# Performance work log

Hardware: AMD Instinct MI355X
Metric: run time of the kernel (lower is better)

The kernel has to match this reference:

```python
import jax, jax.numpy as jnp
import numpy as np

B, S, HID = 2, 2048, 2048
NH, NKV, D = 16, 8, 128
EPS = 1e-6
THETA = 10000.0


def _rms_norm(x, w):
    # RMSNorm over last dim (head_dim), Qwen3-style per-head q/k norm
    var = jnp.mean(jnp.square(x), axis=-1, keepdims=True)
    return x * jax.lax.rsqrt(var + EPS) * w


def _rotate_half(x):
    x1, x2 = jnp.split(x, 2, axis=-1)
    return jnp.concatenate([-x2, x1], axis=-1)


def setup_inputs() -> dict:
    key = jax.random.key(0)
    ks = jax.random.split(key, 8)
    hidden_states = jax.random.normal(ks[0], (B, S, HID), dtype=jnp.float32)
    # rotary embeddings (HF-style: emb = concat(freqs, freqs))
    inv_freq = 1.0 / (THETA ** (jnp.arange(0, D, 2, dtype=jnp.float32) / D))
    pos = jnp.arange(S, dtype=jnp.float32)
    freqs = jnp.outer(pos, inv_freq)                      # [S, D/2]
    emb = jnp.concatenate([freqs, freqs], axis=-1)        # [S, D]
    cos = jnp.broadcast_to(jnp.cos(emb)[None], (B, S, D))
    sin = jnp.broadcast_to(jnp.sin(emb)[None], (B, S, D))
    w_scale = 1.0 / np.sqrt(HID)
    Wq = jax.random.normal(ks[1], (HID, NH * D), dtype=jnp.float32) * w_scale
    Wk = jax.random.normal(ks[2], (HID, NKV * D), dtype=jnp.float32) * w_scale
    Wv = jax.random.normal(ks[3], (HID, NKV * D), dtype=jnp.float32) * w_scale
    Wo = jax.random.normal(ks[4], (NH * D, HID), dtype=jnp.float32) * w_scale
    q_norm_w = jnp.ones((D,), dtype=jnp.float32)
    k_norm_w = jnp.ones((D,), dtype=jnp.float32)
    return {"hidden_states": hidden_states, "cos": cos, "sin": sin,
            "Wq": Wq, "Wk": Wk, "Wv": Wv, "Wo": Wo,
            "q_norm_w": q_norm_w, "k_norm_w": k_norm_w}


def reference(hidden_states, cos, sin, Wq, Wk, Wv, Wo, q_norm_w, k_norm_w):
    b, s, _ = hidden_states.shape
    # projections + per-head RMSNorm on q/k, then [B,H,S,D]
    q = _rms_norm((hidden_states @ Wq).reshape(b, s, NH, D), q_norm_w)
    k = _rms_norm((hidden_states @ Wk).reshape(b, s, NKV, D), k_norm_w)
    v = (hidden_states @ Wv).reshape(b, s, NKV, D)
    q = jnp.swapaxes(q, 1, 2)  # [B,NH,S,D]
    k = jnp.swapaxes(k, 1, 2)  # [B,NKV,S,D]
    v = jnp.swapaxes(v, 1, 2)
    # rotary position embedding
    c = cos[:, None, :, :]
    sn = sin[:, None, :, :]
    q = q * c + _rotate_half(q) * sn
    k = k * c + _rotate_half(k) * sn
    # GQA: expand kv heads to match query heads
    rep = NH // NKV
    k = jnp.repeat(k, rep, axis=1)
    v = jnp.repeat(v, rep, axis=1)
    # scaled causal attention (splash_attention semantics, causal mask)
    q = q * (D ** -0.5)
    scores = jnp.einsum('bhqd,bhkd->bhqk', q, k)
    causal = jnp.tril(jnp.ones((s, s), dtype=bool))
    scores = jnp.where(causal[None, None], scores, jnp.finfo(scores.dtype).min)
    attn = jax.nn.softmax(scores, axis=-1)
    out = jnp.einsum('bhqk,bhkd->bhqd', attn, v)
    out = jnp.swapaxes(out, 1, 2).reshape(b, s, NH * D)
    return out @ Wo
```

## Files before the change

### kernel.cpp

```cpp
#include <hip/hip_runtime.h>
#include <hip/hip_bf16.h>

typedef unsigned short u16;
typedef unsigned int u32;
typedef unsigned long long u64;
typedef __attribute__((ext_vector_type(8))) short short8;
typedef __attribute__((ext_vector_type(4))) float floatx4;

#define AS1 __attribute__((address_space(1)))
#define AS3 __attribute__((address_space(3)))

__device__ __forceinline__ float bf2f(u16 u) {
    u32 x = ((u32)u) << 16;
    float f;
    __builtin_memcpy(&f, &x, 4);
    return f;
}
__device__ __forceinline__ u16 f2bf(float f) {
    u32 x;
    __builtin_memcpy(&x, &f, 4);
    u32 r = (x + 0x7fffu + ((x >> 16) & 1u)) >> 16;
    return (u16)r;
}
__device__ __forceinline__ u32 f2bf_pk(float a, float b) {
    __hip_bfloat162 h = __float22bfloat162_rn(float2{a, b});
    u32 r;
    __builtin_memcpy(&r, &h, 4);
    return r;
}

__global__ __launch_bounds__(256) void convert_x(const float* __restrict__ in,
                                                 u16* __restrict__ out) {
    int i = blockIdx.x * 256 + threadIdx.x;
    float4 v = *(const float4*)(in + (size_t)i * 4);
    u16 o[4] = {f2bf(v.x), f2bf(v.y), f2bf(v.z), f2bf(v.w)};
    *(u64*)(out + (size_t)i * 4) = *(u64*)o;
}

__global__ __launch_bounds__(1024) void transpose_wall(const float* __restrict__ Wq,
                                                       const float* __restrict__ Wk,
                                                       const float* __restrict__ Wv,
                                                       const float* __restrict__ Wo,
                                                       u16* __restrict__ WqkvT,
                                                       u16* __restrict__ WoT) {
    const int z = blockIdx.z;
    const float* in;
    u16* out;
    int C;
    if (z == 0) { in = Wq; out = WqkvT; C = 2048; }
    else if (z == 1) { in = Wk; out = WqkvT + 2048 * 2048; C = 1024; }
    else if (z == 2) { in = Wv; out = WqkvT + 3072 * 2048; C = 1024; }
    else { in = Wo; out = WoT; C = 2048; }
    const int c0 = blockIdx.x * 32, r0 = blockIdx.y * 32;
    if (c0 >= C) return;
    __shared__ u16 t[32][33];
    const int tx = threadIdx.x, ty = threadIdx.y;
    t[ty][tx] = f2bf(in[(size_t)(r0 + ty) * C + c0 + tx]);
    __syncthreads();
    out[(size_t)(c0 + ty) * 2048 + r0 + tx] = t[tx][ty];
}

__global__ __launch_bounds__(1024) void transpose_v(const u16* __restrict__ QKV,
                                                    u16* __restrict__ Vt) {
    __shared__ u16 t[32][33];
    const int tx = threadIdx.x, ty = threadIdx.y;
    const int b = blockIdx.z >> 3, kv = blockIdx.z & 7;
    const int s0 = blockIdx.x * 32, d0 = blockIdx.y * 32;
    t[ty][tx] = QKV[(size_t)(b * 2048 + s0 + ty) * 4096 + 3072 + kv * 128 + d0 + tx];
    __syncthreads();
    Vt[(size_t)((b * 8 + kv) * 128 + d0 + ty) * 2048 + s0 + tx] = t[tx][ty];
}

template <typename OUT_T>
__global__ __launch_bounds__(512, 2) void gemm256(const u16* __restrict__ A,
                                                  const u16* __restrict__ Bt,
                                                  OUT_T* __restrict__ C,
                                                  int M, int N, int K) {
    (void)M;
    __shared__ __align__(16) u16 lds[2][2][2][128 * 64];
    const int tid = threadIdx.x;
    const int wave = tid >> 6, lane = tid & 63;
    const int lr = lane & 15, lq = lane >> 4;
    const int wm = wave >> 2, wn = wave & 3;
    const int m0 = blockIdx.y * 256, n0 = blockIdx.x * 256;

    const int srow = lane >> 3;
    const int schunk = ((lane & 7) ^ srow) << 3;
    const int slot = wave << 1;

    auto stage = [&](const u16* src, int rbase, int buf, int mat, int half, int k0) {
#pragma unroll
        for (int j = 0; j < 2; j++) {
            int r = rbase + half * 128 + (slot + j) * 8 + srow;
            __builtin_amdgcn_global_load_lds(
                (const AS1 void*)(src + (size_t)r * K + k0 + schunk),
                (AS3 void*)(&lds[buf][mat][half][(slot + j) * 512]), 16, 0, 0);
        }
    };

    floatx4 zf = {0.f, 0.f, 0.f, 0.f};
    floatx4 acc[8][4];
#pragma unroll
    for (int i = 0; i < 8; i++)
#pragma unroll
        for (int jn = 0; jn < 4; jn++) acc[i][jn] = zf;

    const int NT = K >> 6;

    stage(Bt, n0, 0, 1, 0, 0);
    stage(Bt, n0, 0, 1, 1, 0);
    stage(A, m0, 0, 0, 0, 0);
    stage(A, m0, 0, 0, 1, 0);
    if (NT > 1) {
        stage(Bt, n0, 1, 1, 0, 64);
        stage(Bt, n0, 1, 1, 1, 64);
        stage(A, m0, 1, 0, 0, 64);
        asm volatile("s_waitcnt vmcnt(6)" ::: "memory");
    } else {
        asm volatile("s_waitcnt vmcnt(0)" ::: "memory");
    }
    __builtin_amdgcn_s_barrier();

    for (int kt = 0; kt < NT; kt++) {
        const int b = kt & 1;
        const u16* Ab = &lds[b][0][wm][0];
        const u16* Bb = &lds[b][1][wn >> 1][0];
        const int brow = (wn & 1) * 64;
        const int sx = lr & 7;
        const int nk = (kt + 2) << 6;

        short8 bf0[4], bf1[4], af[4];
#pragma unroll
        for (int jn = 0; jn < 4; jn++) {
            int rh = brow + jn * 16 + lr;
            bf0[jn] = *(const short8*)(Bb + rh * 64 + ((lq ^ sx) << 3));
            bf1[jn] = *(const short8*)(Bb + rh * 64 + (((4 + lq) ^ sx) << 3));
        }
#pragma unroll
        for (int i = 0; i < 4; i++)
            af[i] = *(const short8*)(Ab + (i * 16 + lr) * 64 + ((lq ^ sx) << 3));
        if (kt + 1 < NT) stage(A, m0, b ^ 1, 0, 1, (kt + 1) << 6);
        __builtin_amdgcn_s_barrier();
        asm volatile("s_waitcnt lgkmcnt(0)" ::: "memory");
        __builtin_amdgcn_sched_barrier(0);
        __builtin_amdgcn_s_setprio(1);
#pragma unroll
        for (int i = 0; i < 4; i++)
#pragma unroll
            for (int jn = 0; jn < 4; jn++)
                acc[i][jn] = __builtin_amdgcn_mfma_f32_16x16x32_bf16(af[i], bf0[jn], acc[i][jn], 0, 0, 0);
        __builtin_amdgcn_s_setprio(0);
        __builtin_amdgcn_s_barrier();

        short8 ag[4];
#pragma unroll
        for (int i = 0; i < 4; i++)
            ag[i] = *(const short8*)(Ab + ((i + 4) * 16 + lr) * 64 + ((lq ^ sx) << 3));
        if (kt + 2 < NT) stage(Bt, n0, b, 1, 0, nk);
        __builtin_amdgcn_s_barrier();
        asm volatile("s_waitcnt lgkmcnt(0)" ::: "memory");
        __builtin_amdgcn_sched_barrier(0);
        __builtin_amdgcn_s_setprio(1);
#pragma unroll
        for (int i = 0; i < 4; i++)
#pragma unroll
            for (int jn = 0; jn < 4; jn++)
                acc[i + 4][jn] = __builtin_amdgcn_mfma_f32_16x16x32_bf16(ag[i], bf0[jn], acc[i + 4][jn], 0, 0, 0);
        __builtin_amdgcn_s_setprio(0);
        __builtin_amdgcn_s_barrier();

        short8 c0[4], c1[4];
#pragma unroll
        for (int i = 0; i < 4; i++) {
            c0[i] = *(const short8*)(Ab + (i * 16 + lr) * 64 + (((4 + lq) ^ sx) << 3));
            c1[i] = *(const short8*)(Ab + ((i + 4) * 16 + lr) * 64 + (((4 + lq) ^ sx) << 3));
        }
        if (kt + 2 < NT) stage(Bt, n0, b, 1, 1, nk);
        __builtin_amdgcn_s_barrier();
        asm volatile("s_waitcnt lgkmcnt(0)" ::: "memory");
        __builtin_amdgcn_sched_barrier(0);
        __builtin_amdgcn_s_setprio(1);
#pragma unroll
        for (int i = 0; i < 4; i++)
#pragma unroll
            for (int jn = 0; jn < 4; jn++)
                acc[i][jn] = __builtin_amdgcn_mfma_f32_16x16x32_bf16(c0[i], bf1[jn], acc[i][jn], 0, 0, 0);
        __builtin_amdgcn_s_setprio(0);
        __builtin_amdgcn_s_barrier();

        if (kt + 2 < NT) stage(A, m0, b, 0, 0, nk);
        __builtin_amdgcn_s_barrier();
        __builtin_amdgcn_s_setprio(1);
#pragma unroll
        for (int i = 0; i < 4; i++)
#pragma unroll
            for (int jn = 0; jn < 4; jn++)
                acc[i + 4][jn] = __builtin_amdgcn_mfma_f32_16x16x32_bf16(c1[i], bf1[jn], acc[i + 4][jn], 0, 0, 0);
        __builtin_amdgcn_s_setprio(0);
        if (kt + 2 < NT) asm volatile("s_waitcnt vmcnt(6)" ::: "memory");
        else asm volatile("s_waitcnt vmcnt(0)" ::: "memory");
        __builtin_amdgcn_s_barrier();
    }

#pragma unroll
    for (int i = 0; i < 8; i++)
#pragma unroll
        for (int jn = 0; jn < 4; jn++)
#pragma unroll
            for (int r = 0; r < 4; r++) {
                int row = m0 + wm * 128 + i * 16 + lq * 4 + r;
                int col = n0 + wn * 64 + jn * 16 + lr;
                if constexpr (sizeof(OUT_T) == 2)
                    C[(size_t)row * N + col] = f2bf(acc[i][jn][r]);
                else
                    C[(size_t)row * N + col] = acc[i][jn][r];
            }
}

__global__ __launch_bounds__(256) void norm_rope(u16* __restrict__ QKV,
                                                 const float* __restrict__ cosb,
                                                 const float* __restrict__ sinb,
                                                 const float* __restrict__ qw,
                                                 const float* __restrict__ kw) {
    const int tid = threadIdx.x;
    const int wave = tid >> 6, lane = tid & 63;
    const int t = blockIdx.x * 4 + wave;
    u16* ptr;
    const float* w;
    float scale;
    int bs;
    if (t < 65536) {
        bs = t >> 4;
        ptr = QKV + (size_t)bs * 4096 + (t & 15) * 128;
        w = qw;
        scale = 0.08838834764831845f * 1.4426950408889634f;
    } else {
        int t2 = t - 65536;
        bs = t2 >> 3;
        ptr = QKV + (size_t)bs * 4096 + 2048 + (t2 & 7) * 128;
        w = kw;
        scale = 1.0f;
    }
    const int d = lane * 2;
    u32 xv = *(const u32*)(ptr + d);
    float x0 = bf2f((u16)(xv & 0xffff)), x1 = bf2f((u16)(xv >> 16));
    float ss = x0 * x0 + x1 * x1;
#pragma unroll
    for (int off = 1; off < 64; off <<= 1) ss += __shfl_xor(ss, off);
    float rn = rsqrtf(ss * (1.0f / 128.0f) + 1e-6f);
    float2 wv = *(const float2*)(w + d);
    float y0 = x0 * rn * wv.x;
    float y1 = x1 * rn * wv.y;
    float p0 = __shfl_xor(y0, 32);
    float p1 = __shfl_xor(y1, 32);
    float sgn = (lane < 32) ? -1.0f : 1.0f;
    float2 cv = *(const float2*)(cosb + (size_t)bs * 128 + d);
    float2 sv = *(const float2*)(sinb + (size_t)bs * 128 + d);
    float o0 = (y0 * cv.x + sgn * p0 * sv.x) * scale;
    float o1 = (y1 * cv.y + sgn * p1 * sv.y) * scale;
    *(u32*)(ptr + d) = (u32)f2bf(o0) | ((u32)f2bf(o1) << 16);
}

__global__ __launch_bounds__(512, 2) void attn_kernel(const u16* __restrict__ QKV,
                                                      const u16* __restrict__ Vt,
                                                      u16* __restrict__ O) {
    __shared__ __align__(16) u16 Ks[2][64 * 128];
    __shared__ __align__(16) u16 Vs[2][128 * 64];
    const int tid = threadIdx.x;
    const int wave = tid >> 6, lane = tid & 63;
    const int lr = lane & 15, lq = lane >> 4;
    const int h = blockIdx.y, b = blockIdx.z;
    const int qt = (b == 0) ? (15 - blockIdx.x) : blockIdx.x;
    const int kv = h >> 1;
    const int q0 = qt * 128;
    const int wq = wave * 16;

    auto stage = [&](int buf, int k0s) {
#pragma unroll
        for (int j = 0; j < 2; j++) {
            int r = wave * 8 + j * 4 + (lane >> 4);
            int c = (lane & 15) ^ (r & 15);
            __builtin_amdgcn_global_load_lds(
                (const AS1 void*)(QKV + (size_t)(b * 2048 + k0s + r) * 4096 + 2048 + kv * 128 + c * 8),
                (AS3 void*)(&Ks[buf][(wave * 8 + j * 4) * 128]), 16, 0, 0);
        }
#pragma unroll
        for (int j = 0; j < 2; j++) {
            int r = wave * 16 + j * 8 + (lane >> 3);
            int c = (lane & 7) ^ (r & 7);
            __builtin_amdgcn_global_load_lds(
                (const AS1 void*)(Vt + (size_t)((b * 8 + kv) * 128 + r) * 2048 + k0s + c * 8),
                (AS3 void*)(&Vs[buf][(wave * 16 + j * 8) * 64]), 16, 0, 0);
        }
    };

    short8 qf[4];
#pragma unroll
    for (int t = 0; t < 4; t++)
        qf[t] = *(const short8*)(QKV + (size_t)(b * 2048 + q0 + wq + lr) * 4096 + h * 128 + t * 32 + lq * 8);

    floatx4 zf = {0.f, 0.f, 0.f, 0.f};
    floatx4 oacc[8];
#pragma unroll
    for (int jn = 0; jn < 8; jn++) oacc[jn] = zf;
    float mstate = -1e30f;
    float lstate = 0.f;

    const int nIter = (qt + 1) * 2;

    stage(0, 0);

    for (int kt = 0; kt < nIter; kt++) {
        const int k0 = kt * 64;
        const int cur = kt & 1;
        __syncthreads();
        if (kt + 1 < nIter) stage(cur ^ 1, k0 + 64);

        if (k0 <= q0 + wq + 15) {
            const u16* KsC = &Ks[cur][0];
            const u16* VsC = &Vs[cur][0];
            floatx4 sacc[4];
#pragma unroll
            for (int jm = 0; jm < 4; jm++) sacc[jm] = zf;
#pragma unroll
            for (int t = 0; t < 4; t++) {
                short8 a[4];
#pragma unroll
                for (int jm = 0; jm < 4; jm++)
                    a[jm] = *(const short8*)(KsC + (jm * 16 + lr) * 128 + (((t * 4 + lq) ^ lr) << 3));
#pragma unroll
                for (int jm = 0; jm < 4; jm++)
                    sacc[jm] = __builtin_amdgcn_mfma_f32_16x16x32_bf16(a[jm], qf[t], sacc[jm], 0, 0, 0);
            }

            if (k0 + 63 > q0 + wq) {
#pragma unroll
                for (int jm = 0; jm < 4; jm++) {
                    int diff = (q0 + wq + lr) - (k0 + jm * 16 + lq * 4);
#pragma unroll
                    for (int r = 0; r < 4; r++)
                        if (r > diff) sacc[jm][r] = -1e30f;
                }
            }

            float mx = -1e30f;
#pragma unroll
            for (int jm = 0; jm < 4; jm++)
#pragma unroll
                for (int r = 0; r < 4; r++) mx = fmaxf(mx, sacc[jm][r]);
            mx = fmaxf(mx, __shfl_xor(mx, 16));
            mx = fmaxf(mx, __shfl_xor(mx, 32));
            float mnew = fmaxf(mstate, mx);
            float alpha = exp2f(mstate - mnew);
            mstate = mnew;
            float rs = 0.f;
#pragma unroll
            for (int jm = 0; jm < 4; jm++)
#pragma unroll
                for (int r = 0; r < 4; r++) {
                    float p = exp2f(sacc[jm][r] - mnew);
                    sacc[jm][r] = p;
                    rs += p;
                }
            rs += __shfl_xor(rs, 16);
            rs += __shfl_xor(rs, 32);
            lstate = lstate * alpha + rs;

            u64 pb[4];
#pragma unroll
            for (int jm = 0; jm < 4; jm++) {
                u32 lo = f2bf_pk(sacc[jm][0], sacc[jm][1]);
                u32 hi = f2bf_pk(sacc[jm][2], sacc[jm][3]);
                pb[jm] = (u64)lo | ((u64)hi << 32);
            }

            float ao[4];
#pragma unroll
            for (int r = 0; r < 4; r++) ao[r] = __shfl(alpha, lq * 4 + r);
#pragma unroll
            for (int jn = 0; jn < 8; jn++)
#pragma unroll
                for (int r = 0; r < 4; r++) oacc[jn][r] *= ao[r];

#pragma unroll
            for (int t = 0; t < 2; t++) {
                union { short8 v; u64 q[2]; } pa;
                pa.q[0] = pb[2 * t];
                pa.q[1] = pb[2 * t + 1];
#pragma unroll
                for (int jn = 0; jn < 8; jn++) {
                    const u16* vrow = VsC + (jn * 16 + lr) * 64 + (lq & 1) * 4;
                    union { short8 v; u64 q[2]; } vb;
                    vb.q[0] = *(const u64*)(vrow + (((t * 4 + (lq >> 1)) ^ (lr & 7)) << 3));
                    vb.q[1] = *(const u64*)(vrow + (((t * 4 + 2 + (lq >> 1)) ^ (lr & 7)) << 3));
                    oacc[jn] = __builtin_amdgcn_mfma_f32_16x16x32_bf16(pa.v, vb.v, oacc[jn], 0, 0, 0);
                }
            }
        }
    }

    float lo[4];
#pragma unroll
    for (int r = 0; r < 4; r++) lo[r] = __shfl(lstate, lq * 4 + r);
#pragma unroll
    for (int jn = 0; jn < 8; jn++)
#pragma unroll
        for (int r = 0; r < 4; r++) {
            int row = q0 + wq + lq * 4 + r;
            O[(size_t)(b * 2048 + row) * 2048 + h * 128 + jn * 16 + lr] =
                f2bf(oacc[jn][r] / lo[r]);
        }
}

extern "C" void kernel_launch(void* const* d_in, const int* in_sizes, int n_in,
                              void* d_out, int out_size, void* d_ws, size_t ws_size,
                              hipStream_t stream) {
    const float* X = (const float*)d_in[0];
    const float* cosb = (const float*)d_in[1];
    const float* sinb = (const float*)d_in[2];
    const float* Wq = (const float*)d_in[3];
    const float* Wk = (const float*)d_in[4];
    const float* Wv = (const float*)d_in[5];
    const float* Wo = (const float*)d_in[6];
    const float* qw = (const float*)d_in[7];
    const float* kw = (const float*)d_in[8];
    float* out = (float*)d_out;
    u16* ws = (u16*)d_ws;

    u16* WqkvT = ws;
    u16* WoT = WqkvT + 8388608;
    u16* Xb = WoT + 4194304;
    u16* QKVb = Xb + 8388608;
    u16* Vtb = QKVb + 16777216;
    u16* Ob = Xb;

    dim3 tb(32, 32);
    transpose_wall<<<dim3(64, 64, 4), tb, 0, stream>>>(Wq, Wk, Wv, Wo, WqkvT, WoT);
    convert_x<<<8192, 256, 0, stream>>>(X, Xb);

    gemm256<u16><<<dim3(16, 16), 512, 0, stream>>>(Xb, WqkvT, QKVb, 4096, 4096, 2048);

    norm_rope<<<24576, 256, 0, stream>>>(QKVb, cosb, sinb, qw, kw);
    transpose_v<<<dim3(64, 4, 16), tb, 0, stream>>>(QKVb, Vtb);

    attn_kernel<<<dim3(16, 16, 2), 512, 0, stream>>>(QKVb, Vtb, Ob);

    gemm256<float><<<dim3(8, 16), 512, 0, stream>>>(Ob, WoT, out, 4096, 2048, 2048);
}
```

Before: 384.4 us.

## Fuse prep kernels, add 256x128 output GEMM, lazy softmax rescale in attention

Merges the X conversion into the weight transpose kernel and the V transpose into the norm/rope kernel, which removes two launches. Replaces the output-projection GEMM with a 256x128 tile variant so 256 blocks launch instead of 128, improving CU coverage on the 2048-wide output. In attention it skips the running-max rescale while the max grows by no more than a threshold, defers the row-sum reductions to the end, and raises wave priority around the MFMA sections. The lazy rescale trades fewer multiplies and shuffles for a bounded exponent growth that could reduce accuracy margin.

```diff
diff --git a/kernel.cpp b/kernel.cpp
--- a/kernel.cpp
+++ b/kernel.cpp
@@ -29,21 +29,26 @@
     return r;
 }
 
-__global__ __launch_bounds__(256) void convert_x(const float* __restrict__ in,
-                                                 u16* __restrict__ out) {
-    int i = blockIdx.x * 256 + threadIdx.x;
-    float4 v = *(const float4*)(in + (size_t)i * 4);
-    u16 o[4] = {f2bf(v.x), f2bf(v.y), f2bf(v.z), f2bf(v.w)};
-    *(u64*)(out + (size_t)i * 4) = *(u64*)o;
-}
-
-__global__ __launch_bounds__(1024) void transpose_wall(const float* __restrict__ Wq,
-                                                       const float* __restrict__ Wk,
-                                                       const float* __restrict__ Wv,
-                                                       const float* __restrict__ Wo,
-                                                       u16* __restrict__ WqkvT,
-                                                       u16* __restrict__ WoT) {
+__global__ __launch_bounds__(1024) void prep_weights(const float* __restrict__ Wq,
+                                                     const float* __restrict__ Wk,
+                                                     const float* __restrict__ Wv,
+                                                     const float* __restrict__ Wo,
+                                                     const float* __restrict__ X,
+                                                     u16* __restrict__ WqkvT,
+                                                     u16* __restrict__ WoT,
+                                                     u16* __restrict__ Xb) {
     const int z = blockIdx.z;
+    const int tx = threadIdx.x, ty = threadIdx.y;
+    if (z == 4) {
+        int idx = blockIdx.y * 64 + blockIdx.x;
+        if (idx >= 2048) return;
+        int tid = ty * 32 + tx;
+        size_t i = (size_t)idx * 4096 + (size_t)tid * 4;
+        float4 v = *(const float4*)(X + i);
+        u16 o[4] = {f2bf(v.x), f2bf(v.y), f2bf(v.z), f2bf(v.w)};
+        *(u64*)(Xb + i) = *(u64*)o;
+        return;
+    }
     const float* in;
     u16* out;
     int C;
@@ -54,21 +59,9 @@
     const int c0 = blockIdx.x * 32, r0 = blockIdx.y * 32;
     if (c0 >= C) return;
     __shared__ u16 t[32][33];
-    const int tx = threadIdx.x, ty = threadIdx.y;
     t[ty][tx] = f2bf(in[(size_t)(r0 + ty) * C + c0 + tx]);
     __syncthreads();
     out[(size_t)(c0 + ty) * 2048 + r0 + tx] = t[tx][ty];
-}
-
-__global__ __launch_bounds__(1024) void transpose_v(const u16* __restrict__ QKV,
-                                                    u16* __restrict__ Vt) {
-    __shared__ u16 t[32][33];
-    const int tx = threadIdx.x, ty = threadIdx.y;
-    const int b = blockIdx.z >> 3, kv = blockIdx.z & 7;
-    const int s0 = blockIdx.x * 32, d0 = blockIdx.y * 32;
-    t[ty][tx] = QKV[(size_t)(b * 2048 + s0 + ty) * 4096 + 3072 + kv * 128 + d0 + tx];
-    __syncthreads();
-    Vt[(size_t)((b * 8 + kv) * 128 + d0 + ty) * 2048 + s0 + tx] = t[tx][ty];
 }
 
 template <typename OUT_T>
@@ -217,14 +210,174 @@
             }
 }
 
-__global__ __launch_bounds__(256) void norm_rope(u16* __restrict__ QKV,
-                                                 const float* __restrict__ cosb,
-                                                 const float* __restrict__ sinb,
-                                                 const float* __restrict__ qw,
-                                                 const float* __restrict__ kw) {
+template <typename OUT_T>
+__global__ __launch_bounds__(512, 2) void gemm128n(const u16* __restrict__ A,
+                                                   const u16* __restrict__ Bt,
+                                                   OUT_T* __restrict__ C,
+                                                   int M, int N, int K) {
+    (void)M;
+    __shared__ __align__(16) u16 Abuf[2][2][128 * 64];
+    __shared__ __align__(16) u16 Bbuf[2][128 * 64];
     const int tid = threadIdx.x;
     const int wave = tid >> 6, lane = tid & 63;
-    const int t = blockIdx.x * 4 + wave;
+    const int lr = lane & 15, lq = lane >> 4;
+    const int wm = wave >> 1, wn = wave & 1;
+    const int m0 = blockIdx.y * 256, n0 = blockIdx.x * 128;
+
+    const int srow = lane >> 3;
+    const int schunk = ((lane & 7) ^ srow) << 3;
+    const int slot = wave << 1;
+
+    auto stage = [&](const u16* src, int rowbase, u16* ldsbase, int k0) {
+#pragma unroll
+        for (int j = 0; j < 2; j++) {
+            int r = rowbase + (slot + j) * 8 + srow;
+            __builtin_amdgcn_global_load_lds(
+                (const AS1 void*)(src + (size_t)r * K + k0 + schunk),
+                (AS3 void*)(ldsbase + (slot + j) * 512), 16, 0, 0);
+        }
+    };
+
+    floatx4 zf = {0.f, 0.f, 0.f, 0.f};
+    floatx4 acc[4][4];
+#pragma unroll
+    for (int i = 0; i < 4; i++)
+#pragma unroll
+        for (int jn = 0; jn < 4; jn++) acc[i][jn] = zf;
+
+    const int NT = K >> 6;
+
+    stage(A, m0, &Abuf[0][0][0], 0);
+    stage(A, m0 + 128, &Abuf[0][1][0], 0);
+    stage(Bt, n0, &Bbuf[0][0], 0);
+    if (NT > 1) {
+        stage(A, m0, &Abuf[1][0][0], 64);
+        stage(Bt, n0, &Bbuf[1][0], 64);
+        asm volatile("s_waitcnt vmcnt(4)" ::: "memory");
+    } else {
+        asm volatile("s_waitcnt vmcnt(0)" ::: "memory");
+    }
+    __builtin_amdgcn_s_barrier();
+
+    for (int kt = 0; kt < NT; kt++) {
+        const int b = kt & 1;
+        const u16* Ab = &Abuf[b][wm >> 1][0];
+        const u16* Bb = &Bbuf[b][0];
+        const int ar = (wm & 1) * 64;
+        const int br = wn * 64;
+        const int sx = lr & 7;
+        const int nk = (kt + 2) << 6;
+
+        short8 bf0[4], bf1[4], af[4];
+#pragma unroll
+        for (int jn = 0; jn < 4; jn++) {
+            int rh = br + jn * 16 + lr;
+            bf0[jn] = *(const short8*)(Bb + rh * 64 + ((lq ^ sx) << 3));
+            bf1[jn] = *(const short8*)(Bb + rh * 64 + (((4 + lq) ^ sx) << 3));
+        }
+#pragma unroll
+        for (int i = 0; i < 4; i++)
+            af[i] = *(const short8*)(Ab + (ar + i * 16 + lr) * 64 + ((lq ^ sx) << 3));
+        if (kt + 1 < NT) stage(A, m0 + 128, &Abuf[b ^ 1][1][0], (kt + 1) << 6);
+        __builtin_amdgcn_s_barrier();
+        asm volatile("s_waitcnt lgkmcnt(0)" ::: "memory");
+        __builtin_amdgcn_sched_barrier(0);
+        __builtin_amdgcn_s_setprio(1);
+#pragma unroll
+        for (int i = 0; i < 2; i++)
+#pragma unroll
+            for (int jn = 0; jn < 4; jn++)
+                acc[i][jn] = __builtin_amdgcn_mfma_f32_16x16x32_bf16(af[i], bf0[jn], acc[i][jn], 0, 0, 0);
+        __builtin_amdgcn_s_setprio(0);
+        __builtin_amdgcn_s_barrier();
+
+        if (kt + 2 < NT) stage(Bt, n0, &Bbuf[b][0], nk);
+        __builtin_amdgcn_s_barrier();
+        __builtin_amdgcn_s_setprio(1);
+#pragma unroll
+        for (int i = 2; i < 4; i++)
+#pragma unroll
+            for (int jn = 0; jn < 4; jn++)
+                acc[i][jn] = __builtin_amdgcn_mfma_f32_16x16x32_bf16(af[i], bf0[jn], acc[i][jn], 0, 0, 0);
+        __builtin_amdgcn_s_setprio(0);
+        __builtin_amdgcn_s_barrier();
+
+        short8 ag[4];
+#pragma unroll
+        for (int i = 0; i < 4; i++)
+            ag[i] = *(const short8*)(Ab + (ar + i * 16 + lr) * 64 + (((4 + lq) ^ sx) << 3));
+        __builtin_amdgcn_s_barrier();
+        asm volatile("s_waitcnt lgkmcnt(0)" ::: "memory");
+        __builtin_amdgcn_sched_barrier(0);
+        __builtin_amdgcn_s_setprio(1);
+#pragma unroll
+        for (int i = 0; i < 2; i++)
+#pragma unroll
+            for (int jn = 0; jn < 4; jn++)
+                acc[i][jn] = __builtin_amdgcn_mfma_f32_16x16x32_bf16(ag[i], bf1[jn], acc[i][jn], 0, 0, 0);
+        __builtin_amdgcn_s_setprio(0);
+        __builtin_amdgcn_s_barrier();
+
+        if (kt + 2 < NT) stage(A, m0, &Abuf[b][0][0], nk);
+        __builtin_amdgcn_s_barrier();
+        __builtin_amdgcn_s_setprio(1);
+#pragma unroll
+        for (int i = 2; i < 4; i++)
+#pragma unroll
+            for (int jn = 0; jn < 4; jn++)
+                acc[i][jn] = __builtin_amdgcn_mfma_f32_16x16x32_bf16(ag[i], bf1[jn], acc[i][jn], 0, 0, 0);
+        __builtin_amdgcn_s_setprio(0);
+        if (kt + 2 < NT) asm volatile("s_waitcnt vmcnt(4)" ::: "memory");
+        else asm volatile("s_waitcnt vmcnt(0)" ::: "memory");
+        __builtin_amdgcn_s_barrier();
+    }
+
+#pragma unroll
+    for (int i = 0; i < 4; i++)
+#pragma unroll
+        for (int jn = 0; jn < 4; jn++)
+#pragma unroll
+            for (int r = 0; r < 4; r++) {
+                int row = m0 + wm * 64 + i * 16 + lq * 4 + r;
+                int col = n0 + wn * 64 + jn * 16 + lr;
+                if constexpr (sizeof(OUT_T) == 2)
+                    C[(size_t)row * N + col] = f2bf(acc[i][jn][r]);
+                else
+                    C[(size_t)row * N + col] = acc[i][jn][r];
+            }
+}
+
+__global__ __launch_bounds__(256) void prep_qkv(u16* __restrict__ QKV,
+                                                u16* __restrict__ Vt,
+                                                const float* __restrict__ cosb,
+                                                const float* __restrict__ sinb,
+                                                const float* __restrict__ qw,
+                                                const float* __restrict__ kw) {
+    const int bx = blockIdx.x;
+    const int tid = threadIdx.x;
+    if (bx >= 24576) {
+        const int idx = bx - 24576;
+        const int s0 = (idx & 63) * 32;
+        const int d0 = ((idx >> 6) & 3) * 32;
+        const int zz = idx >> 8;
+        const int b = zz >> 3, kv = zz & 7;
+        __shared__ u16 t[32][33];
+        const int tx = tid & 31, ty0 = tid >> 5;
+#pragma unroll
+        for (int p = 0; p < 4; p++) {
+            int r = ty0 + p * 8;
+            t[r][tx] = QKV[(size_t)(b * 2048 + s0 + r) * 4096 + 3072 + kv * 128 + d0 + tx];
+        }
+        __syncthreads();
+#pragma unroll
+        for (int p = 0; p < 4; p++) {
+            int r = ty0 + p * 8;
+            Vt[(size_t)((b * 8 + kv) * 128 + d0 + r) * 2048 + s0 + tx] = t[tx][r];
+        }
+        return;
+    }
+    const int wave = tid >> 6, lane = tid & 63;
+    const int t = bx * 4 + wave;
     u16* ptr;
     const float* w;
     float scale;
@@ -322,6 +475,7 @@
             floatx4 sacc[4];
 #pragma unroll
             for (int jm = 0; jm < 4; jm++) sacc[jm] = zf;
+            __builtin_amdgcn_s_setprio(1);
 #pragma unroll
             for (int t = 0; t < 4; t++) {
                 short8 a[4];
@@ -332,6 +486,7 @@
                 for (int jm = 0; jm < 4; jm++)
                     sacc[jm] = __builtin_amdgcn_mfma_f32_16x16x32_bf16(a[jm], qf[t], sacc[jm], 0, 0, 0);
             }
+            __builtin_amdgcn_s_setprio(0);
 
             if (k0 + 63 > q0 + wq) {
 #pragma unroll
@@ -345,14 +500,17 @@
 
             float mx = -1e30f;
 #pragma unroll
-            for (int jm = 0; jm < 4; jm++)
-#pragma unroll
-                for (int r = 0; r < 4; r++) mx = fmaxf(mx, sacc[jm][r]);
+            for (int jm = 0; jm < 4; jm++) {
+                float a0 = fmaxf(sacc[jm][0], sacc[jm][1]);
+                float a1 = fmaxf(sacc[jm][2], sacc[jm][3]);
+                mx = fmaxf(mx, fmaxf(a0, a1));
+            }
             mx = fmaxf(mx, __shfl_xor(mx, 16));
             mx = fmaxf(mx, __shfl_xor(mx, 32));
-            float mnew = fmaxf(mstate, mx);
-            float alpha = exp2f(mstate - mnew);
-            mstate = mnew;
+
+            bool defer = __all(mx - mstate <= 8.0f);
+            float mnew = defer ? mstate : fmaxf(mstate, mx);
+
             float rs = 0.f;
 #pragma unroll
             for (int jm = 0; jm < 4; jm++)
@@ -362,9 +520,20 @@
                     sacc[jm][r] = p;
                     rs += p;
                 }
-            rs += __shfl_xor(rs, 16);
-            rs += __shfl_xor(rs, 32);
-            lstate = lstate * alpha + rs;
+
+            if (!defer) {
+                float alpha = exp2f(mstate - mnew);
+                mstate = mnew;
+                lstate *= alpha;
+                float ao[4];
+#pragma unroll
+                for (int r = 0; r < 4; r++) ao[r] = __shfl(alpha, lq * 4 + r);
+#pragma unroll
+                for (int jn = 0; jn < 8; jn++)
+#pragma unroll
+                    for (int r = 0; r < 4; r++) oacc[jn][r] *= ao[r];
+            }
+            lstate += rs;
 
             u64 pb[4];
 #pragma unroll
@@ -374,14 +543,7 @@
                 pb[jm] = (u64)lo | ((u64)hi << 32);
             }
 
-            float ao[4];
-#pragma unroll
-            for (int r = 0; r < 4; r++) ao[r] = __shfl(alpha, lq * 4 + r);
-#pragma unroll
-            for (int jn = 0; jn < 8; jn++)
-#pragma unroll
-                for (int r = 0; r < 4; r++) oacc[jn][r] *= ao[r];
-
+            __builtin_amdgcn_s_setprio(1);
 #pragma unroll
             for (int t = 0; t < 2; t++) {
                 union { short8 v; u64 q[2]; } pa;
@@ -396,9 +558,12 @@
                     oacc[jn] = __builtin_amdgcn_mfma_f32_16x16x32_bf16(pa.v, vb.v, oacc[jn], 0, 0, 0);
                 }
             }
-        }
-    }
-
+            __builtin_amdgcn_s_setprio(0);
+        }
+    }
+
+    lstate += __shfl_xor(lstate, 16);
+    lstate += __shfl_xor(lstate, 32);
     float lo[4];
 #pragma unroll
     for (int r = 0; r < 4; r++) lo[r] = __shfl(lstate, lq * 4 + r);
@@ -434,16 +599,14 @@
     u16* Vtb = QKVb + 16777216;
     u16* Ob = Xb;
 
-    dim3 tb(32, 32);
-    transpose_wall<<<dim3(64, 64, 4), tb, 0, stream>>>(Wq, Wk, Wv, Wo, WqkvT, WoT);
-    convert_x<<<8192, 256, 0, stream>>>(X, Xb);
+    prep_weights<<<dim3(64, 64, 5), dim3(32, 32), 0, stream>>>(Wq, Wk, Wv, Wo, X,
+                                                               WqkvT, WoT, Xb);
 
     gemm256<u16><<<dim3(16, 16), 512, 0, stream>>>(Xb, WqkvT, QKVb, 4096, 4096, 2048);
 
-    norm_rope<<<24576, 256, 0, stream>>>(QKVb, cosb, sinb, qw, kw);
-    transpose_v<<<dim3(64, 4, 16), tb, 0, stream>>>(QKVb, Vtb);
+    prep_qkv<<<28672, 256, 0, stream>>>(QKVb, Vtb, cosb, sinb, qw, kw);
 
     attn_kernel<<<dim3(16, 16, 2), 512, 0, stream>>>(QKVb, Vtb, Ob);
 
-    gemm256<float><<<dim3(8, 16), 512, 0, stream>>>(Ob, WoT, out, 4096, 2048, 2048);
-}
+    gemm128n<float><<<dim3(16, 16), 512, 0, stream>>>(Ob, WoT, out, 4096, 2048, 2048);
+}
```

Result: faster. 366.7 us (-4.6%).
